# Kernel tuning notes

Hardware: AMD Instinct MI355X
Metric: run time of the kernel (lower is better)

Reference implementation:

```python
import jax, jax.numpy as jnp
import numpy as np

NEG_SLOPE = 0.2  # PyG GATConv default negative_slope


def _edges(B, C):
    # Fully-connected (no self) edges among the FIRST C nodes only (as in original
    # code, which ignores batch when building edge_index), plus self loops on all
    # B*C nodes (PyG GATConv add_self_loops=True default).
    N = B * C
    ij = np.array([(i, j) for i in range(C) for j in range(C) if i != j], dtype=np.int32)
    loops = np.arange(N, dtype=np.int32)
    src = jnp.concatenate([jnp.asarray(ij[:, 0]), jnp.asarray(loops)])
    dst = jnp.concatenate([jnp.asarray(ij[:, 1]), jnp.asarray(loops)])
    return src, dst, N


def _gat_conv(x2d, W, att_src, att_dst, bias, src, dst, N):
    h = x2d @ W                              # [N, Fout] linear projection (no bias)
    a_src = h @ att_src                      # [N] per-node src attention logit
    a_dst = h @ att_dst                      # [N] per-node dst attention logit
    e = jax.nn.leaky_relu(a_src[src] + a_dst[dst], NEG_SLOPE)   # [E] edge scores
    m = jax.ops.segment_max(e, dst, num_segments=N)             # segment softmax
    ex = jnp.exp(e - m[dst])
    denom = jax.ops.segment_sum(ex, dst, num_segments=N)
    alpha = ex / denom[dst]                                     # [E]
    out = jax.ops.segment_sum(alpha[:, None] * h[src], dst, num_segments=N)
    return out + bias


def setup_inputs() -> dict:
    key = jax.random.key(0)
    k1, k2, k3, k4 = jax.random.split(key, 4)
    B, C, Fin, Fout = 2048, 63, 250, 250
    x = jax.random.normal(k1, (B, 1, C, Fin), dtype=jnp.float32)
    W = jax.random.normal(k2, (Fin, Fout), dtype=jnp.float32) / np.sqrt(Fin).astype(np.float32)
    att_src = jax.random.normal(k3, (Fout,), dtype=jnp.float32) / np.sqrt(Fout).astype(np.float32)
    att_dst = jax.random.normal(k4, (Fout,), dtype=jnp.float32) / np.sqrt(Fout).astype(np.float32)
    bias = jnp.zeros((Fout,), dtype=jnp.float32)
    return {"x": x, "W": W, "att_src": att_src, "att_dst": att_dst, "bias": bias}


def reference(x, W, att_src, att_dst, bias):
    B, _, C, F = x.shape
    src, dst, N = _edges(B, C)
    out = _gat_conv(x.reshape(N, F), W, att_src, att_dst, bias, src, dst, N)
    return out.reshape(B, 1, C, -1)   # [B, 1, C, Fout]
```

## Files before the change

### kernel.cpp

```cpp
#include <hip/hip_runtime.h>
#include <hip/hip_bf16.h>

#define FIN 250
#define NROWS 129024
#define NSTRIPES (NROWS / 16)
#define TOTXF (NROWS * FIN)
#define NBLOCKS 224
#define WAVES_PER_BLOCK 12
#define NWAVES_TOT (NBLOCKS * WAVES_PER_BLOCK)
#define NTASKS (NSTRIPES * 2)

typedef short short8 __attribute__((ext_vector_type(8)));
typedef float f32x4 __attribute__((ext_vector_type(4)));

__device__ __forceinline__ short f2bf(float f) {
    __bf16 b = (__bf16)f;
    return __builtin_bit_cast(short, b);
}

__device__ __forceinline__ void do_task(const float* __restrict__ x,
                                        const unsigned short* wt,
                                        float* __restrict__ out,
                                        int stripe, int half, int m, int kg,
                                        unsigned bswz, const float (&bcol)[8]) {
    float2 tmp[32];
    unsigned fbase = (unsigned)(stripe * 16 + m) * FIN + (unsigned)(kg * 8);
    #pragma unroll
    for (int kk = 0; kk < 8; ++kk) {
        #pragma unroll
        for (int p = 0; p < 4; ++p) {
            unsigned idx = fbase + (unsigned)(kk * 32 + p * 2);
            idx = idx > (TOTXF - 2u) ? (TOTXF - 2u) : idx;
            tmp[kk * 4 + p] = *(const float2*)(x + idx);
        }
    }
    short8 af[8];
    #pragma unroll
    for (int kk = 0; kk < 8; ++kk) {
        #pragma unroll
        for (int p = 0; p < 4; ++p) {
            af[kk][2 * p]     = f2bf(tmp[kk * 4 + p].x);
            af[kk][2 * p + 1] = f2bf(tmp[kk * 4 + p].y);
        }
    }
    const f32x4 zero = {0.f, 0.f, 0.f, 0.f};
    f32x4 acc[8];
    #pragma unroll
    for (int nf = 0; nf < 8; ++nf) acc[nf] = zero;

    const unsigned chbase = (unsigned)(half * 128) * 512u;
    #pragma unroll
    for (int kk = 0; kk < 8; ++kk) {
        #pragma unroll
        for (int nf = 0; nf < 8; ++nf) {
            unsigned off = chbase + (unsigned)(nf * 16 + m) * 512u
                         + (((unsigned)(kk * 64 + kg * 16)) ^ bswz);
            short8 bf = *(const short8*)((const char*)wt + off);
            acc[nf] = __builtin_amdgcn_mfma_f32_16x16x32_bf16(af[kk], bf, acc[nf], 0, 0, 0);
        }
    }
    unsigned obase = (unsigned)(stripe * 16 + kg * 4) * FIN
                   + (unsigned)(half * 128 + m);
    #pragma unroll
    for (int nf = 0; nf < 8; ++nf) {
        if (half == 0 || nf < 7 || m < 10) {
            #pragma unroll
            for (int j = 0; j < 4; ++j) {
                out[obase + (unsigned)(j * FIN) + (unsigned)(nf * 16)] = acc[nf][j] + bcol[nf];
            }
        }
    }
}

__global__ void __launch_bounds__(768, 3)
gat_gemm(const float* __restrict__ x, const float* __restrict__ W,
         const float* __restrict__ bias, float* __restrict__ out)
{
    __shared__ __align__(16) unsigned short wt[256 * 256];

    const int tid = threadIdx.x;

    {
        uint4* p = (uint4*)wt;
        uint4 z = make_uint4(0u, 0u, 0u, 0u);
        for (int i = tid; i < 8192; i += 768) p[i] = z;
    }
    __syncthreads();

    for (int idx = tid; idx < FIN * FIN; idx += 768) {
        unsigned k = (unsigned)idx / FIN;
        unsigned c = (unsigned)idx - k * FIN;
        unsigned off = (c << 9) + ((2u * k) ^ ((c & 7u) << 4));
        *(unsigned short*)((char*)wt + off) = (unsigned short)f2bf(W[idx]);
    }
    __syncthreads();

    const int lane = tid & 63;
    const int m    = lane & 15;
    const int kg   = lane >> 4;
    const unsigned bswz = ((unsigned)(m & 7)) << 4;
    const int gw   = blockIdx.x * WAVES_PER_BLOCK + (tid >> 6);

    float bcol0[8], bcol1[8];
    #pragma unroll
    for (int nf = 0; nf < 8; ++nf) {
        int c0 = nf * 16 + m;
        int c1 = 128 + nf * 16 + m;
        bcol0[nf] = bias[c0];
        bcol1[nf] = (c1 < FIN) ? bias[c1] : 0.f;
    }

    for (int t = gw; t < NTASKS; t += NWAVES_TOT) {
        int stripe = t >> 1;
        int half   = t & 1;
        if (half == 0)
            do_task(x, wt, out, stripe, 0, m, kg, bswz, bcol0);
        else
            do_task(x, wt, out, stripe, 1, m, kg, bswz, bcol1);
    }
}

__global__ void __launch_bounds__(1024, 1)
gat_attn(const float* __restrict__ att_src, const float* __restrict__ att_dst,
         float* __restrict__ out)
{
    __shared__ float hs[63 * 252];
    __shared__ float asrc[64], adst[64];
    __shared__ float alpha[63 * 64];

    const int tid = threadIdx.x;

    for (int idx = tid; idx < 63 * FIN; idx += 1024) {
        int r = idx / FIN, f = idx - r * FIN;
        hs[r * 252 + f] = out[idx];
    }
    __syncthreads();

    {
        int r = tid >> 4, t = tid & 15;
        float s1 = 0.f, s2 = 0.f;
        if (r < 63) {
            for (int k = t; k < FIN; k += 16) {
                float h = hs[r * 252 + k];
                s1 += h * att_src[k];
                s2 += h * att_dst[k];
            }
        }
        #pragma unroll
        for (int o = 8; o >= 1; o >>= 1) {
            s1 += __shfl_xor(s1, o, 16);
            s2 += __shfl_xor(s2, o, 16);
        }
        if (r < 63 && t == 0) { asrc[r] = s1; adst[r] = s2; }
    }
    __syncthreads();

    {
        int d = tid >> 4, t = tid & 15;
        if (d < 63) {
            float ad = adst[d];
            float e_[4];
            float mx = -1e30f;
            #pragma unroll
            for (int q = 0; q < 4; ++q) {
                int s = t + q * 16;
                float e = -1e30f;
                if (s < 63) {
                    e = asrc[s] + ad;
                    e = e > 0.f ? e : 0.2f * e;
                }
                e_[q] = e;
                mx = fmaxf(mx, e);
            }
            #pragma unroll
            for (int o = 8; o >= 1; o >>= 1) mx = fmaxf(mx, __shfl_xor(mx, o, 16));
            float den = 0.f;
            #pragma unroll
            for (int q = 0; q < 4; ++q) {
                int s = t + q * 16;
                float ex = (s < 63) ? __expf(e_[q] - mx) : 0.f;
                e_[q] = ex;
                den += ex;
            }
            #pragma unroll
            for (int o = 8; o >= 1; o >>= 1) den += __shfl_xor(den, o, 16);
            float rd = 1.f / den;
            #pragma unroll
            for (int q = 0; q < 4; ++q) {
                int s = t + q * 16;
                if (s < 63) alpha[d * 64 + s] = e_[q] * rd;
            }
        }
    }
    __syncthreads();

    for (int idx = tid; idx < 63 * FIN; idx += 1024) {
        int d = idx / FIN, f = idx - d * FIN;
        float v = 0.f;
        for (int s = 0; s < 63; ++s)
            v += alpha[d * 64 + s] * hs[s * 252 + f];
        out[idx] = v;
    }
}

extern "C" void kernel_launch(void* const* d_in, const int* in_sizes, int n_in,
                              void* d_out, int out_size, void* d_ws, size_t ws_size,
                              hipStream_t stream) {
    (void)in_sizes; (void)n_in; (void)d_ws; (void)ws_size; (void)out_size;
    const float* x        = (const float*)d_in[0];
    const float* W        = (const float*)d_in[1];
    const float* att_src  = (const float*)d_in[2];
    const float* att_dst  = (const float*)d_in[3];
    const float* bias     = (const float*)d_in[4];
    float* out            = (float*)d_out;

    gat_gemm<<<NBLOCKS, 768, 0, stream>>>(x, W, bias, out);
    gat_attn<<<1, 1024, 0, stream>>>(att_src, att_dst, out);
}
```

Baseline: 100.2 us.

## Software-pipeline x stripe loads and reuse A fragments across both column halves

Measured after the change: 121.2 us. 20.9% more time.

```diff
diff --git a/kernel.cpp b/kernel.cpp
--- a/kernel.cpp
+++ b/kernel.cpp
@@ -5,10 +5,9 @@
 #define NROWS 129024
 #define NSTRIPES (NROWS / 16)
 #define TOTXF (NROWS * FIN)
-#define NBLOCKS 224
+#define NBLOCKS 256
 #define WAVES_PER_BLOCK 12
 #define NWAVES_TOT (NBLOCKS * WAVES_PER_BLOCK)
-#define NTASKS (NSTRIPES * 2)
 
 typedef short short8 __attribute__((ext_vector_type(8)));
 typedef float f32x4 __attribute__((ext_vector_type(4)));
@@ -18,12 +17,20 @@
     return __builtin_bit_cast(short, b);
 }
 
-__device__ __forceinline__ void do_task(const float* __restrict__ x,
-                                        const unsigned short* wt,
-                                        float* __restrict__ out,
-                                        int stripe, int half, int m, int kg,
-                                        unsigned bswz, const float (&bcol)[8]) {
-    float2 tmp[32];
+__device__ __forceinline__ void load_stripe_fast(float2 (&buf)[32], const float* __restrict__ x,
+                                                 int stripe, int m, int kg) {
+    const float* base = x + (unsigned)(stripe * 16 + m) * FIN + (unsigned)(kg * 8);
+    #pragma unroll
+    for (int kk = 0; kk < 8; ++kk) {
+        #pragma unroll
+        for (int p = 0; p < 4; ++p) {
+            buf[kk * 4 + p] = *(const float2*)(base + kk * 32 + p * 2);
+        }
+    }
+}
+
+__device__ __forceinline__ void load_stripe_safe(float2 (&buf)[32], const float* __restrict__ x,
+                                                 int stripe, int m, int kg) {
     unsigned fbase = (unsigned)(stripe * 16 + m) * FIN + (unsigned)(kg * 8);
     #pragma unroll
     for (int kk = 0; kk < 8; ++kk) {
@@ -31,18 +38,16 @@
         for (int p = 0; p < 4; ++p) {
             unsigned idx = fbase + (unsigned)(kk * 32 + p * 2);
             idx = idx > (TOTXF - 2u) ? (TOTXF - 2u) : idx;
-            tmp[kk * 4 + p] = *(const float2*)(x + idx);
-        }
-    }
-    short8 af[8];
-    #pragma unroll
-    for (int kk = 0; kk < 8; ++kk) {
-        #pragma unroll
-        for (int p = 0; p < 4; ++p) {
-            af[kk][2 * p]     = f2bf(tmp[kk * 4 + p].x);
-            af[kk][2 * p + 1] = f2bf(tmp[kk * 4 + p].y);
-        }
-    }
+            buf[kk * 4 + p] = *(const float2*)(x + idx);
+        }
+    }
+}
+
+__device__ __forceinline__ void mfma_half(const short8 (&af)[8],
+                                          const unsigned short* wt,
+                                          float* __restrict__ out,
+                                          int stripe, int half, int m, int kg,
+                                          unsigned bswz, const float (&bcol)[16]) {
     const f32x4 zero = {0.f, 0.f, 0.f, 0.f};
     f32x4 acc[8];
     #pragma unroll
@@ -59,14 +64,14 @@
             acc[nf] = __builtin_amdgcn_mfma_f32_16x16x32_bf16(af[kk], bf, acc[nf], 0, 0, 0);
         }
     }
-    unsigned obase = (unsigned)(stripe * 16 + kg * 4) * FIN
-                   + (unsigned)(half * 128 + m);
+    unsigned obase = (unsigned)(stripe * 16 + kg * 4) * FIN + (unsigned)(half * 128 + m);
     #pragma unroll
     for (int nf = 0; nf < 8; ++nf) {
         if (half == 0 || nf < 7 || m < 10) {
+            float b = bcol[half * 8 + nf];
             #pragma unroll
             for (int j = 0; j < 4; ++j) {
-                out[obase + (unsigned)(j * FIN) + (unsigned)(nf * 16)] = acc[nf][j] + bcol[nf];
+                out[obase + (unsigned)(j * FIN) + (unsigned)(nf * 16)] = acc[nf][j] + b;
             }
         }
     }
@@ -101,22 +106,39 @@
     const unsigned bswz = ((unsigned)(m & 7)) << 4;
     const int gw   = blockIdx.x * WAVES_PER_BLOCK + (tid >> 6);
 
-    float bcol0[8], bcol1[8];
-    #pragma unroll
-    for (int nf = 0; nf < 8; ++nf) {
-        int c0 = nf * 16 + m;
-        int c1 = 128 + nf * 16 + m;
-        bcol0[nf] = bias[c0];
-        bcol1[nf] = (c1 < FIN) ? bias[c1] : 0.f;
-    }
-
-    for (int t = gw; t < NTASKS; t += NWAVES_TOT) {
-        int stripe = t >> 1;
-        int half   = t & 1;
-        if (half == 0)
-            do_task(x, wt, out, stripe, 0, m, kg, bswz, bcol0);
-        else
-            do_task(x, wt, out, stripe, 1, m, kg, bswz, bcol1);
+    float bcol[16];
+    #pragma unroll
+    for (int nf = 0; nf < 16; ++nf) {
+        int c = nf * 16 + m;
+        bcol[nf] = (c < FIN) ? bias[c] : 0.f;
+    }
+
+    float2 buf[32];
+    short8 af[8];
+
+    int s = gw;
+    if (s >= NSTRIPES) return;
+    if (s < NSTRIPES - 1) load_stripe_fast(buf, x, s, m, kg);
+    else                  load_stripe_safe(buf, x, s, m, kg);
+
+    for (;;) {
+        #pragma unroll
+        for (int kk = 0; kk < 8; ++kk) {
+            #pragma unroll
+            for (int p = 0; p < 4; ++p) {
+                af[kk][2 * p]     = f2bf(buf[kk * 4 + p].x);
+                af[kk][2 * p + 1] = f2bf(buf[kk * 4 + p].y);
+            }
+        }
+        int snext = s + NWAVES_TOT;
+        if (snext < NSTRIPES - 1)      load_stripe_fast(buf, x, snext, m, kg);
+        else if (snext == NSTRIPES - 1) load_stripe_safe(buf, x, snext, m, kg);
+
+        mfma_half(af, wt, out, s, 0, m, kg, bswz, bcol);
+        mfma_half(af, wt, out, s, 1, m, kg, bswz, bcol);
+
+        if (snext >= NSTRIPES) break;
+        s = snext;
     }
 }
 
@@ -163,10 +185,10 @@
             float mx = -1e30f;
             #pragma unroll
             for (int q = 0; q < 4; ++q) {
-                int s = t + q * 16;
+                int sdx = t + q * 16;
                 float e = -1e30f;
-                if (s < 63) {
-                    e = asrc[s] + ad;
+                if (sdx < 63) {
+                    e = asrc[sdx] + ad;
                     e = e > 0.f ? e : 0.2f * e;
                 }
                 e_[q] = e;
@@ -177,8 +199,8 @@
             float den = 0.f;
             #pragma unroll
             for (int q = 0; q < 4; ++q) {
-                int s = t + q * 16;
-                float ex = (s < 63) ? __expf(e_[q] - mx) : 0.f;
+                int sdx = t + q * 16;
+                float ex = (sdx < 63) ? __expf(e_[q] - mx) : 0.f;
                 e_[q] = ex;
                 den += ex;
             }
@@ -187,8 +209,8 @@
             float rd = 1.f / den;
             #pragma unroll
             for (int q = 0; q < 4; ++q) {
-                int s = t + q * 16;
-                if (s < 63) alpha[d * 64 + s] = e_[q] * rd;
+                int sdx = t + q * 16;
+                if (sdx < 63) alpha[d * 64 + sdx] = e_[q] * rd;
             }
         }
     }
@@ -197,8 +219,8 @@
     for (int idx = tid; idx < 63 * FIN; idx += 1024) {
         int d = idx / FIN, f = idx - d * FIN;
         float v = 0.f;
-        for (int s = 0; s < 63; ++s)
-            v += alpha[d * 64 + s] * hs[s * 252 + f];
+        for (int sdx = 0; sdx < 63; ++sdx)
+            v += alpha[d * 64 + sdx] * hs[sdx * 252 + f];
         out[idx] = v;
     }
 }
```
